# Kernel optimization log

Hardware: AMD Instinct MI355X
Metric: run time of the kernel (lower is better)

Reference implementation:

```python
import jax, jax.numpy as jnp
import numpy as np

DIM = 512
DIM_HEAD = 64
HEADS = 8
INNER = DIM_HEAD * HEADS  # 512
OUT_DIM = DIM
PB_ALPHA = 128.0
EPS = 1e-5
SCALE = DIM_HEAD ** (-0.5) / PB_ALPHA


def layer_norm(x, g):
    mean = jnp.mean(x, axis=-1, keepdims=True)
    var = jnp.mean(jnp.square(x - mean), axis=-1, keepdims=True)  # unbiased=False
    return (x - mean) * jax.lax.rsqrt(var + EPS) * g


def setup_inputs() -> dict:
    key = jax.random.key(0)
    ks = jax.random.split(key, 6)
    b, n, r = 4, 64, 256
    x = jax.random.normal(ks[0], (b, n, r, DIM), dtype=jnp.float32)
    g_norm = jnp.ones((DIM,), dtype=jnp.float32)
    W_q = jax.random.normal(ks[1], (DIM, INNER), dtype=jnp.float32) * (DIM ** -0.5)
    W_kv = jax.random.normal(ks[2], (DIM, 2 * DIM_HEAD), dtype=jnp.float32) * (DIM ** -0.5)
    W_out = jax.random.normal(ks[3], (INNER, OUT_DIM), dtype=jnp.float32) * (INNER ** -0.5)
    g_out = jnp.ones((OUT_DIM,), dtype=jnp.float32)
    return {"x": x, "g_norm": g_norm, "W_q": W_q, "W_kv": W_kv, "W_out": W_out, "g_out": g_out}


def reference(x, g_norm, W_q, W_kv, W_out, g_out):
    b, n, r, _ = x.shape
    xn = layer_norm(x, g_norm)                      # [b,n,r,dim]
    q = xn @ W_q                                    # [b,n,r,h*d]
    kv = xn @ W_kv                                  # context defaults to x
    k, v = jnp.split(kv, 2, axis=-1)                # [b,n,r,d] each, shared over heads
    q = q.reshape(b, n, r, HEADS, DIM_HEAD).transpose(0, 1, 3, 2, 4)  # b n h i d
    q = q * SCALE
    sim = jnp.einsum('bnhid,bnjd->bnhij', q, k)
    sim = (sim - jax.lax.stop_gradient(jnp.max(sim, axis=-1, keepdims=True))) * PB_ALPHA
    attn = jax.nn.softmax(sim, axis=-1)
    out = jnp.einsum('bnhij,bnjd->bnhid', attn, v)  # b n h i d
    out = out.transpose(0, 1, 3, 2, 4).reshape(b, n, r, INNER)  # b n i (h d)
    out = out @ W_out
    return layer_norm(out, g_out)
```

## Files before the change

kernel.cpp:

```cpp
#include <hip/hip_runtime.h>
#include <stdint.h>


#define DIM   512
#define DHEAD 64
#define RLEN  256
#define TOK   65536

typedef __bf16 bf16;
typedef __bf16 bf16x4 __attribute__((ext_vector_type(4)));
typedef __bf16 bf16x8 __attribute__((ext_vector_type(8)));
typedef float  f32x4  __attribute__((ext_vector_type(4)));
typedef short  s16x4  __attribute__((ext_vector_type(4)));

__device__ __forceinline__ f32x4 mfma16(bf16x8 a, bf16x8 b, f32x4 c) {
  return __builtin_amdgcn_mfma_f32_16x16x32_bf16(a, b, c, 0, 0, 0);
}
__device__ __forceinline__ f32x4 mfma_k16(bf16x4 a, bf16x4 b, f32x4 c) {
#if __has_builtin(__builtin_amdgcn_mfma_f32_16x16x16bf16_1k)
  return __builtin_amdgcn_mfma_f32_16x16x16bf16_1k(
      __builtin_bit_cast(s16x4, a), __builtin_bit_cast(s16x4, b), c, 0, 0, 0);
#else
  f32x4 d = c;
  asm volatile("v_mfma_f32_16x16x16_bf16 %0, %1, %2, %0"
               : "+v"(d) : "v"(a), "v"(b));
  return d;
#endif
}
__device__ __forceinline__ f32x4 fzero4() {
  f32x4 z; z[0] = z[1] = z[2] = z[3] = 0.f; return z;
}
__device__ __forceinline__ void gload_lds16(const void* g, void* l) {
  __builtin_amdgcn_global_load_lds(
      (const __attribute__((address_space(1))) void*)g,
      (__attribute__((address_space(3))) void*)l, 16, 0, 0);
}

__global__ __launch_bounds__(256) void k_prep_ln(
    const float* __restrict__ Wq, const float* __restrict__ Wkv,
    const float* __restrict__ Wout,
    const float* __restrict__ x, const float* __restrict__ gnorm,
    bf16* __restrict__ wall, bf16* __restrict__ woutt, bf16* __restrict__ xn) {
  if (blockIdx.x < 144) {
    __shared__ bf16 tile[64][72];
    const int b = blockIdx.x, tid = threadIdx.x;
    const float* src; bf16* dst; int srcN, kt, nt;
    if (b < 64)       { src = Wq;   dst = wall;  srcN = 512; kt = b >> 3;        nt = b & 7; }
    else if (b < 128) { src = Wout; dst = woutt; srcN = 512; kt = (b - 64) >> 3; nt = (b - 64) & 7; }
    else              { src = Wkv;  dst = wall + (size_t)512 * DIM; srcN = 128;
                        kt = (b - 128) >> 1; nt = (b - 128) & 1; }
    const int k0 = kt * 64, n0 = nt * 64;
    #pragma unroll
    for (int i = 0; i < 4; ++i) {
      int idx = i * 256 + tid;
      int r = idx >> 4, c4 = (idx & 15) * 4;
      float4 v = *(const float4*)(src + (size_t)(k0 + r) * srcN + n0 + c4);
      tile[r][c4 + 0] = (bf16)v.x;
      tile[r][c4 + 1] = (bf16)v.y;
      tile[r][c4 + 2] = (bf16)v.z;
      tile[r][c4 + 3] = (bf16)v.w;
    }
    __syncthreads();
    #pragma unroll
    for (int i = 0; i < 2; ++i) {
      int idx = i * 256 + tid;
      int n = idx >> 3, c = (idx & 7) * 8;
      bf16x8 o;
      #pragma unroll
      for (int j = 0; j < 8; ++j) o[j] = tile[c + j][n];
      *(bf16x8*)(dst + (size_t)(n0 + n) * DIM + k0 + c) = o;
    }
    return;
  }
  const int lane = threadIdx.x & 63;
  const int gw = (blockIdx.x - 144) * 4 + (threadIdx.x >> 6);
  float gv[8];
  #pragma unroll
  for (int j = 0; j < 8; ++j) gv[j] = gnorm[lane * 8 + j];
  #pragma unroll
  for (int i = 0; i < 8; ++i) {
    size_t row = (size_t)gw * 8 + i;
    const float4* xp = (const float4*)(x + row * DIM + lane * 8);
    float4 v0 = xp[0], v1 = xp[1];
    float s  = v0.x + v0.y + v0.z + v0.w + v1.x + v1.y + v1.z + v1.w;
    float sq = v0.x*v0.x + v0.y*v0.y + v0.z*v0.z + v0.w*v0.w
             + v1.x*v1.x + v1.y*v1.y + v1.z*v1.z + v1.w*v1.w;
    #pragma unroll
    for (int d = 1; d < 64; d <<= 1) { s += __shfl_xor(s, d); sq += __shfl_xor(sq, d); }
    float mean = s * (1.f / 512.f);
    float var  = sq * (1.f / 512.f) - mean * mean;
    float rs   = rsqrtf(var + 1e-5f);
    bf16x8 o;
    o[0] = (bf16)((v0.x - mean) * rs * gv[0]);
    o[1] = (bf16)((v0.y - mean) * rs * gv[1]);
    o[2] = (bf16)((v0.z - mean) * rs * gv[2]);
    o[3] = (bf16)((v0.w - mean) * rs * gv[3]);
    o[4] = (bf16)((v1.x - mean) * rs * gv[4]);
    o[5] = (bf16)((v1.y - mean) * rs * gv[5]);
    o[6] = (bf16)((v1.z - mean) * rs * gv[6]);
    o[7] = (bf16)((v1.w - mean) * rs * gv[7]);
    *(bf16x8*)(xn + row * DIM + lane * 8) = o;
  }
}

__global__ __launch_bounds__(256) void k_gemm_qkv(
    const bf16* __restrict__ xn, const bf16* __restrict__ wall,
    bf16* __restrict__ qbuf, bf16* __restrict__ kbuf, bf16* __restrict__ vtbuf) {
  __shared__ bf16 sa[2][128 * 32];
  __shared__ bf16 sb[2][128 * 32];
  const int t = threadIdx.x, wave = t >> 6, lane = t & 63;
  const int l15 = lane & 15, g = lane >> 4;
  const int wm = wave >> 1, wn = wave & 1;
  int wg = (blockIdx.x & 7) * 320 + (blockIdx.x >> 3);
  const int bm = wg / 5, bn = wg % 5;
  const char* Abase = (const char*)(xn   + (size_t)bm * 128 * DIM);
  const char* Bbase = (const char*)(wall + (size_t)bn * 128 * DIM);
  const int srow0 = wave * 16 + (lane >> 2);
  const int skb   = (lane & 3) * 16;

  #pragma unroll
  for (int c = 0; c < 2; ++c) {
    int row = c * 64 + srow0;
    int kb = skb ^ ((row & 3) << 4);
    gload_lds16(Abase + (size_t)row * 1024 + kb, (char*)&sa[0][0] + c * 4096 + wave * 1024);
    gload_lds16(Bbase + (size_t)row * 1024 + kb, (char*)&sb[0][0] + c * 4096 + wave * 1024);
  }
  __syncthreads();

  f32x4 acc[4][4];
  #pragma unroll
  for (int mi = 0; mi < 4; ++mi)
    #pragma unroll
    for (int ni = 0; ni < 4; ++ni) acc[mi][ni] = fzero4();

  #pragma unroll 2
  for (int step = 0; step < 16; ++step) {
    const int cur = step & 1;
    if (step < 15) {
      int kk2 = (step + 1) * 64;
      #pragma unroll
      for (int c = 0; c < 2; ++c) {
        int row = c * 64 + srow0;
        int kb = skb ^ ((row & 3) << 4);
        gload_lds16(Abase + (size_t)row * 1024 + kk2 + kb,
                    (char*)&sa[cur ^ 1][0] + c * 4096 + wave * 1024);
        gload_lds16(Bbase + (size_t)row * 1024 + kk2 + kb,
                    (char*)&sb[cur ^ 1][0] + c * 4096 + wave * 1024);
      }
    }
    bf16x8 a[4], b[4];
    #pragma unroll
    for (int mi = 0; mi < 4; ++mi) {
      int row = wm * 64 + mi * 16 + l15;
      a[mi] = *(const bf16x8*)((const char*)&sa[cur][0] + row * 64 + ((g * 16) ^ ((row & 3) << 4)));
    }
    #pragma unroll
    for (int ni = 0; ni < 4; ++ni) {
      int row = wn * 64 + ni * 16 + l15;
      b[ni] = *(const bf16x8*)((const char*)&sb[cur][0] + row * 64 + ((g * 16) ^ ((row & 3) << 4)));
    }
    #pragma unroll
    for (int mi = 0; mi < 4; ++mi)
      #pragma unroll
      for (int ni = 0; ni < 4; ++ni)
        acc[mi][ni] = mfma16(a[mi], b[ni], acc[mi][ni]);
    __syncthreads();
  }

  const float QSC = 0.1803368801f;
  #pragma unroll
  for (int ni = 0; ni < 4; ++ni) {
    int col0 = bn * 128 + wn * 64 + ni * 16;
    if (col0 < 512) {
      bf16* dst = qbuf + col0 + l15;
      #pragma unroll
      for (int mi = 0; mi < 4; ++mi)
        #pragma unroll
        for (int jj = 0; jj < 4; ++jj) {
          size_t row = (size_t)bm * 128 + wm * 64 + mi * 16 + g * 4 + jj;
          dst[row * DIM] = (bf16)(acc[mi][ni][jj] * QSC);
        }
    } else if (col0 < 576) {
      bf16* dst = kbuf + (col0 - 512) + l15;
      #pragma unroll
      for (int mi = 0; mi < 4; ++mi)
        #pragma unroll
        for (int jj = 0; jj < 4; ++jj) {
          size_t row = (size_t)bm * 128 + wm * 64 + mi * 16 + g * 4 + jj;
          dst[row * DHEAD] = (bf16)acc[mi][ni][jj];
        }
    } else {
      int d = col0 - 576 + l15;
      #pragma unroll
      for (int mi = 0; mi < 4; ++mi) {
        size_t row = (size_t)bm * 128 + wm * 64 + mi * 16 + g * 4;
        int bnr = (int)(row >> 8), kv = (int)(row & 255);
        bf16x4 v4;
        v4[0] = (bf16)acc[mi][ni][0]; v4[1] = (bf16)acc[mi][ni][1];
        v4[2] = (bf16)acc[mi][ni][2]; v4[3] = (bf16)acc[mi][ni][3];
        *(bf16x4*)(vtbuf + (size_t)bnr * 16384 + (size_t)d * 256 + kv) = v4;
      }
    }
  }
}

__global__ __launch_bounds__(512) void k_out_fused(
    const bf16* __restrict__ abuf, const bf16* __restrict__ woutt,
    const float* __restrict__ gout, float* __restrict__ out) {
  __shared__ bf16 sa[2][64 * 32];
  __shared__ bf16 sb[2][512 * 32];
  __shared__ float2 part[64][4];
  __shared__ float2 stats[64];
  const int t = threadIdx.x, wave = t >> 6, lane = t & 63;
  const int l15 = lane & 15, g = lane >> 4;
  const int wm = wave >> 2, wn = wave & 3;
  int wg = (blockIdx.x & 7) * 128 + (blockIdx.x >> 3);
  const size_t row0 = (size_t)wg * 64;
  const char* Abase = (const char*)(abuf + row0 * DIM);
  const int nsub = wave * 16 + (lane >> 2);
  const int skb  = (lane & 3) * 16;

  #pragma unroll
  for (int c = 0; c < 4; ++c) {
    int row = c * 128 + nsub;
    int kb = skb ^ ((row & 3) << 4);
    gload_lds16((const char*)(woutt + (size_t)row * DIM) + kb,
                (char*)&sb[0][0] + c * 8192 + wave * 1024);
  }
  if (t < 256) {
    int kb = skb ^ ((nsub & 3) << 4);
    gload_lds16(Abase + (size_t)nsub * 1024 + kb,
                (char*)&sa[0][0] + wave * 1024 + (lane & 63) * 16);
  }
  __syncthreads();

  f32x4 acc[2][8];
  #pragma unroll
  for (int mi = 0; mi < 2; ++mi)
    #pragma unroll
    for (int ni = 0; ni < 8; ++ni) acc[mi][ni] = fzero4();

  #pragma unroll 2
  for (int step = 0; step < 16; ++step) {
    const int cur = step & 1;
    if (step < 15) {
      int kk2 = (step + 1) * 64;
      #pragma unroll
      for (int c = 0; c < 4; ++c) {
        int row = c * 128 + nsub;
        int kb = skb ^ ((row & 3) << 4);
        gload_lds16((const char*)(woutt + (size_t)row * DIM) + kk2 + kb,
                    (char*)&sb[cur ^ 1][0] + c * 8192 + wave * 1024);
      }
      if (t < 256) {
        int kb = skb ^ ((nsub & 3) << 4);
        gload_lds16(Abase + (size_t)nsub * 1024 + kk2 + kb,
                    (char*)&sa[cur ^ 1][0] + wave * 1024 + lane * 16);
      }
    }
    bf16x8 a[2];
    #pragma unroll
    for (int mi = 0; mi < 2; ++mi) {
      int row = wm * 32 + mi * 16 + l15;
      a[mi] = *(const bf16x8*)((const char*)&sa[cur][0] + row * 64 + ((g * 16) ^ ((row & 3) << 4)));
    }
    #pragma unroll
    for (int ni = 0; ni < 8; ++ni) {
      int row = wn * 128 + ni * 16 + l15;
      bf16x8 b = *(const bf16x8*)((const char*)&sb[cur][0] + row * 64 + ((g * 16) ^ ((row & 3) << 4)));
      acc[0][ni] = mfma16(a[0], b, acc[0][ni]);
      acc[1][ni] = mfma16(a[1], b, acc[1][ni]);
    }
    __syncthreads();
  }

  #pragma unroll
  for (int mi = 0; mi < 2; ++mi)
    #pragma unroll
    for (int jj = 0; jj < 4; ++jj) {
      float s = 0.f, q = 0.f;
      #pragma unroll
      for (int ni = 0; ni < 8; ++ni) {
        float v = acc[mi][ni][jj];
        s += v; q += v * v;
      }
      s += __shfl_xor(s, 1); q += __shfl_xor(q, 1);
      s += __shfl_xor(s, 2); q += __shfl_xor(q, 2);
      s += __shfl_xor(s, 4); q += __shfl_xor(q, 4);
      s += __shfl_xor(s, 8); q += __shfl_xor(q, 8);
      if (l15 == 0) part[wm * 32 + mi * 16 + g * 4 + jj][wn] = make_float2(s, q);
    }
  __syncthreads();
  if (t < 64) {
    float S = 0.f, Q = 0.f;
    #pragma unroll
    for (int w = 0; w < 4; ++w) { S += part[t][w].x; Q += part[t][w].y; }
    float mean = S * (1.f / 512.f);
    float var  = Q * (1.f / 512.f) - mean * mean;
    stats[t] = make_float2(mean, rsqrtf(var + 1e-5f));
  }
  __syncthreads();

  #pragma unroll
  for (int mi = 0; mi < 2; ++mi)
    #pragma unroll
    for (int ni = 0; ni < 8; ++ni) {
      int col = wn * 128 + ni * 16 + l15;
      float gg = gout[col];
      #pragma unroll
      for (int jj = 0; jj < 4; ++jj) {
        int row = wm * 32 + mi * 16 + g * 4 + jj;
        float2 st = stats[row];
        out[(row0 + row) * DIM + col] = (acc[mi][ni][jj] - st.x) * st.y * gg;
      }
    }
}

__global__ __launch_bounds__(512, 2) void k_attn(
    bf16* __restrict__ qbuf, const bf16* __restrict__ kbuf,
    const bf16* __restrict__ vtbuf) {
  __shared__ char lds[256 * 144 + 64 * 528];
  char* lk  = lds;
  char* lvt = lds + 256 * 144;
  const int t = threadIdx.x, lane = t & 63;
  const int l15 = lane & 15, g = lane >> 4;
  int wg = (blockIdx.x & 7) * 256 + (blockIdx.x >> 3);
  const int bn = wg >> 3, h = wg & 7;
  const size_t tok0 = (size_t)bn * RLEN;
  const int m0 = (t >> 6) * 32;

  bf16x8 aq[2][2];
  {
    const bf16* qb = qbuf + (tok0 + m0 + l15) * DIM + h * DHEAD + g * 8;
    #pragma unroll
    for (int qh = 0; qh < 2; ++qh)
      #pragma unroll
      for (int ks = 0; ks < 2; ++ks)
        aq[qh][ks] = *(const bf16x8*)(qb + (size_t)qh * 16 * DIM + ks * 32);
  }
  {
    const bf16* ksrc = kbuf + tok0 * DHEAD;
    const bf16* vsrc = vtbuf + (size_t)bn * (64 * 256);
    bf16x8 kr[4], vr[4];
    #pragma unroll
    for (int i = 0; i < 4; ++i) kr[i] = *(const bf16x8*)(ksrc + (i * 512 + t) * 8);
    #pragma unroll
    for (int i = 0; i < 4; ++i) vr[i] = *(const bf16x8*)(vsrc + (i * 512 + t) * 8);
    #pragma unroll
    for (int i = 0; i < 4; ++i) {
      int off = i * 512 + t;
      *(bf16x8*)(lk + (off >> 3) * 144 + (off & 7) * 16) = kr[i];
    }
    #pragma unroll
    for (int i = 0; i < 4; ++i) {
      int off = i * 512 + t;
      *(bf16x8*)(lvt + (off >> 5) * 528 + (off & 31) * 16) = vr[i];
    }
  }
  __syncthreads();

  const char* bk_base = lk  + l15 * 144 + g * 16;
  const char* bv_base = lvt + l15 * 528 + g * 8;

  f32x4 o2[2][4];
  #pragma unroll
  for (int qh = 0; qh < 2; ++qh)
    #pragma unroll
    for (int di = 0; di < 4; ++di) o2[qh][di] = fzero4();
  float lsum0 = 0.f, lsum1 = 0.f;

  __builtin_amdgcn_s_setprio(1);
  #pragma unroll
  for (int f = 0; f < 16; ++f) {
    bf16x8 bk0 = *(const bf16x8*)(bk_base + f * 2304);
    bf16x8 bk1 = *(const bf16x8*)(bk_base + f * 2304 + 64);
    f32x4 s0 = mfma16(bk0, aq[0][0], fzero4());
    s0 = mfma16(bk1, aq[0][1], s0);
    f32x4 s1 = mfma16(bk0, aq[1][0], fzero4());
    s1 = mfma16(bk1, aq[1][1], s1);
    float p00 = exp2f(s0[0]), p01 = exp2f(s0[1]);
    float p02 = exp2f(s0[2]), p03 = exp2f(s0[3]);
    float p10 = exp2f(s1[0]), p11 = exp2f(s1[1]);
    float p12 = exp2f(s1[2]), p13 = exp2f(s1[3]);
    lsum0 += (p00 + p01) + (p02 + p03);
    lsum1 += (p10 + p11) + (p12 + p13);
    bf16x4 pk0, pk1;
    pk0[0] = (bf16)p00; pk0[1] = (bf16)p01; pk0[2] = (bf16)p02; pk0[3] = (bf16)p03;
    pk1[0] = (bf16)p10; pk1[1] = (bf16)p11; pk1[2] = (bf16)p12; pk1[3] = (bf16)p13;
    #pragma unroll
    for (int di = 0; di < 4; ++di) {
      bf16x4 bv = *(const bf16x4*)(bv_base + di * 8448 + f * 32);
      o2[0][di] = mfma_k16(pk0, bv, o2[0][di]);
      o2[1][di] = mfma_k16(pk1, bv, o2[1][di]);
    }
  }
  __builtin_amdgcn_s_setprio(0);

  float linv[2];
  lsum0 += __shfl_xor(lsum0, 16); lsum0 += __shfl_xor(lsum0, 32);
  lsum1 += __shfl_xor(lsum1, 16); lsum1 += __shfl_xor(lsum1, 32);
  linv[0] = 1.0f / lsum0;
  linv[1] = 1.0f / lsum1;

  #pragma unroll
  for (int qh = 0; qh < 2; ++qh)
    #pragma unroll
    for (int jj = 0; jj < 4; ++jj) {
      float inv = __shfl(linv[qh], 4 * g + jj);
      size_t row = tok0 + m0 + qh * 16 + 4 * g + jj;
      #pragma unroll
      for (int di = 0; di < 4; ++di)
        qbuf[row * DIM + h * DHEAD + di * 16 + l15] = (bf16)(o2[qh][di][jj] * inv);
    }
}

extern "C" void kernel_launch(void* const* d_in, const int* in_sizes, int n_in,
                              void* d_out, int out_size, void* d_ws, size_t ws_size,
                              hipStream_t stream) {
  const float* x     = (const float*)d_in[0];
  const float* gnorm = (const float*)d_in[1];
  const float* Wq    = (const float*)d_in[2];
  const float* Wkv   = (const float*)d_in[3];
  const float* Wout  = (const float*)d_in[4];
  const float* gout  = (const float*)d_in[5];
  float* out = (float*)d_out;
  char* ws = (char*)d_ws;
  bf16* wall  = (bf16*)(ws);
  bf16* woutt = (bf16*)(ws + 655360);
  bf16* xnbuf = (bf16*)(ws + 1179648);
  bf16* qbuf  = (bf16*)(ws + 1179648 + (size_t)TOK * DIM * 2);
  bf16* kbuf  = (bf16*)((char*)qbuf + (size_t)TOK * DIM * 2);
  bf16* vtbuf = (bf16*)((char*)kbuf + (size_t)TOK * DHEAD * 2);

  k_prep_ln  <<<dim3(2192), dim3(256), 0, stream>>>(Wq, Wkv, Wout, x, gnorm,
                                                    wall, woutt, xnbuf);
  k_gemm_qkv <<<dim3(2560), dim3(256), 0, stream>>>(xnbuf, wall, qbuf, kbuf, vtbuf);
  k_attn     <<<dim3(2048), dim3(512), 0, stream>>>(qbuf, kbuf, vtbuf);
  k_out_fused<<<dim3(1024), dim3(512), 0, stream>>>(qbuf, woutt, gout, out);
}
```

Baseline: 236.6 us.

## Process four heads per attention block and change LDS swizzle pattern

```diff
diff --git a/kernel.cpp b/kernel.cpp
--- a/kernel.cpp
+++ b/kernel.cpp
@@ -6,6 +6,7 @@
 #define DHEAD 64
 #define RLEN  256
 #define TOK   65536
+#define SWZ(row) ((((row) >> 1) & 3) << 4)
 
 typedef __bf16 bf16;
 typedef __bf16 bf16x4 __attribute__((ext_vector_type(4)));
@@ -121,7 +122,7 @@
   #pragma unroll
   for (int c = 0; c < 2; ++c) {
     int row = c * 64 + srow0;
-    int kb = skb ^ ((row & 3) << 4);
+    int kb = skb ^ SWZ(row);
     gload_lds16(Abase + (size_t)row * 1024 + kb, (char*)&sa[0][0] + c * 4096 + wave * 1024);
     gload_lds16(Bbase + (size_t)row * 1024 + kb, (char*)&sb[0][0] + c * 4096 + wave * 1024);
   }
@@ -141,7 +142,7 @@
       #pragma unroll
       for (int c = 0; c < 2; ++c) {
         int row = c * 64 + srow0;
-        int kb = skb ^ ((row & 3) << 4);
+        int kb = skb ^ SWZ(row);
         gload_lds16(Abase + (size_t)row * 1024 + kk2 + kb,
                     (char*)&sa[cur ^ 1][0] + c * 4096 + wave * 1024);
         gload_lds16(Bbase + (size_t)row * 1024 + kk2 + kb,
@@ -152,12 +153,12 @@
     #pragma unroll
     for (int mi = 0; mi < 4; ++mi) {
       int row = wm * 64 + mi * 16 + l15;
-      a[mi] = *(const bf16x8*)((const char*)&sa[cur][0] + row * 64 + ((g * 16) ^ ((row & 3) << 4)));
+      a[mi] = *(const bf16x8*)((const char*)&sa[cur][0] + row * 64 + ((g * 16) ^ SWZ(row)));
     }
     #pragma unroll
     for (int ni = 0; ni < 4; ++ni) {
       int row = wn * 64 + ni * 16 + l15;
-      b[ni] = *(const bf16x8*)((const char*)&sb[cur][0] + row * 64 + ((g * 16) ^ ((row & 3) << 4)));
+      b[ni] = *(const bf16x8*)((const char*)&sb[cur][0] + row * 64 + ((g * 16) ^ SWZ(row)));
     }
     #pragma unroll
     for (int mi = 0; mi < 4; ++mi)
@@ -223,12 +224,12 @@
   #pragma unroll
   for (int c = 0; c < 4; ++c) {
     int row = c * 128 + nsub;
-    int kb = skb ^ ((row & 3) << 4);
+    int kb = skb ^ SWZ(row);
     gload_lds16((const char*)(woutt + (size_t)row * DIM) + kb,
                 (char*)&sb[0][0] + c * 8192 + wave * 1024);
   }
   if (t < 256) {
-    int kb = skb ^ ((nsub & 3) << 4);
+    int kb = skb ^ SWZ(nsub);
     gload_lds16(Abase + (size_t)nsub * 1024 + kb,
                 (char*)&sa[0][0] + wave * 1024 + (lane & 63) * 16);
   }
@@ -248,12 +249,12 @@
       #pragma unroll
       for (int c = 0; c < 4; ++c) {
         int row = c * 128 + nsub;
-        int kb = skb ^ ((row & 3) << 4);
+        int kb = skb ^ SWZ(row);
         gload_lds16((const char*)(woutt + (size_t)row * DIM) + kk2 + kb,
                     (char*)&sb[cur ^ 1][0] + c * 8192 + wave * 1024);
       }
       if (t < 256) {
-        int kb = skb ^ ((nsub & 3) << 4);
+        int kb = skb ^ SWZ(nsub);
         gload_lds16(Abase + (size_t)nsub * 1024 + kk2 + kb,
                     (char*)&sa[cur ^ 1][0] + wave * 1024 + lane * 16);
       }
@@ -262,12 +263,12 @@
     #pragma unroll
     for (int mi = 0; mi < 2; ++mi) {
       int row = wm * 32 + mi * 16 + l15;
-      a[mi] = *(const bf16x8*)((const char*)&sa[cur][0] + row * 64 + ((g * 16) ^ ((row & 3) << 4)));
+      a[mi] = *(const bf16x8*)((const char*)&sa[cur][0] + row * 64 + ((g * 16) ^ SWZ(row)));
     }
     #pragma unroll
     for (int ni = 0; ni < 8; ++ni) {
       int row = wn * 128 + ni * 16 + l15;
-      bf16x8 b = *(const bf16x8*)((const char*)&sb[cur][0] + row * 64 + ((g * 16) ^ ((row & 3) << 4)));
+      bf16x8 b = *(const bf16x8*)((const char*)&sb[cur][0] + row * 64 + ((g * 16) ^ SWZ(row)));
       acc[0][ni] = mfma16(a[0], b, acc[0][ni]);
       acc[1][ni] = mfma16(a[1], b, acc[1][ni]);
     }
@@ -324,20 +325,11 @@
   char* lvt = lds + 256 * 144;
   const int t = threadIdx.x, lane = t & 63;
   const int l15 = lane & 15, g = lane >> 4;
-  int wg = (blockIdx.x & 7) * 256 + (blockIdx.x >> 3);
-  const int bn = wg >> 3, h = wg & 7;
+  int wg = (blockIdx.x & 7) * 64 + (blockIdx.x >> 3);
+  const int bn = wg >> 1, h0 = (wg & 1) * 4;
   const size_t tok0 = (size_t)bn * RLEN;
   const int m0 = (t >> 6) * 32;
 
-  bf16x8 aq[2][2];
-  {
-    const bf16* qb = qbuf + (tok0 + m0 + l15) * DIM + h * DHEAD + g * 8;
-    #pragma unroll
-    for (int qh = 0; qh < 2; ++qh)
-      #pragma unroll
-      for (int ks = 0; ks < 2; ++ks)
-        aq[qh][ks] = *(const bf16x8*)(qb + (size_t)qh * 16 * DIM + ks * 32);
-  }
   {
     const bf16* ksrc = kbuf + tok0 * DHEAD;
     const bf16* vsrc = vtbuf + (size_t)bn * (64 * 256);
@@ -361,57 +353,72 @@
 
   const char* bk_base = lk  + l15 * 144 + g * 16;
   const char* bv_base = lvt + l15 * 528 + g * 8;
-
-  f32x4 o2[2][4];
-  #pragma unroll
-  for (int qh = 0; qh < 2; ++qh)
-    #pragma unroll
-    for (int di = 0; di < 4; ++di) o2[qh][di] = fzero4();
-  float lsum0 = 0.f, lsum1 = 0.f;
-
-  __builtin_amdgcn_s_setprio(1);
-  #pragma unroll
-  for (int f = 0; f < 16; ++f) {
-    bf16x8 bk0 = *(const bf16x8*)(bk_base + f * 2304);
-    bf16x8 bk1 = *(const bf16x8*)(bk_base + f * 2304 + 64);
-    f32x4 s0 = mfma16(bk0, aq[0][0], fzero4());
-    s0 = mfma16(bk1, aq[0][1], s0);
-    f32x4 s1 = mfma16(bk0, aq[1][0], fzero4());
-    s1 = mfma16(bk1, aq[1][1], s1);
-    float p00 = exp2f(s0[0]), p01 = exp2f(s0[1]);
-    float p02 = exp2f(s0[2]), p03 = exp2f(s0[3]);
-    float p10 = exp2f(s1[0]), p11 = exp2f(s1[1]);
-    float p12 = exp2f(s1[2]), p13 = exp2f(s1[3]);
-    lsum0 += (p00 + p01) + (p02 + p03);
-    lsum1 += (p10 + p11) + (p12 + p13);
-    bf16x4 pk0, pk1;
-    pk0[0] = (bf16)p00; pk0[1] = (bf16)p01; pk0[2] = (bf16)p02; pk0[3] = (bf16)p03;
-    pk1[0] = (bf16)p10; pk1[1] = (bf16)p11; pk1[2] = (bf16)p12; pk1[3] = (bf16)p13;
-    #pragma unroll
-    for (int di = 0; di < 4; ++di) {
-      bf16x4 bv = *(const bf16x4*)(bv_base + di * 8448 + f * 32);
-      o2[0][di] = mfma_k16(pk0, bv, o2[0][di]);
-      o2[1][di] = mfma_k16(pk1, bv, o2[1][di]);
-    }
-  }
-  __builtin_amdgcn_s_setprio(0);
-
-  float linv[2];
-  lsum0 += __shfl_xor(lsum0, 16); lsum0 += __shfl_xor(lsum0, 32);
-  lsum1 += __shfl_xor(lsum1, 16); lsum1 += __shfl_xor(lsum1, 32);
-  linv[0] = 1.0f / lsum0;
-  linv[1] = 1.0f / lsum1;
-
-  #pragma unroll
-  for (int qh = 0; qh < 2; ++qh)
-    #pragma unroll
-    for (int jj = 0; jj < 4; ++jj) {
-      float inv = __shfl(linv[qh], 4 * g + jj);
-      size_t row = tok0 + m0 + qh * 16 + 4 * g + jj;
-      #pragma unroll
-      for (int di = 0; di < 4; ++di)
-        qbuf[row * DIM + h * DHEAD + di * 16 + l15] = (bf16)(o2[qh][di][jj] * inv);
-    }
+  const bf16* qrow = qbuf + (tok0 + m0 + l15) * DIM + g * 8;
+
+  #pragma unroll
+  for (int hi = 0; hi < 4; ++hi) {
+    const int h = h0 + hi;
+    bf16x8 aq[2][2];
+    {
+      const bf16* qb = qrow + h * DHEAD;
+      #pragma unroll
+      for (int qh = 0; qh < 2; ++qh)
+        #pragma unroll
+        for (int ks = 0; ks < 2; ++ks)
+          aq[qh][ks] = *(const bf16x8*)(qb + (size_t)qh * 16 * DIM + ks * 32);
+    }
+
+    f32x4 o2[2][4];
+    #pragma unroll
+    for (int qh = 0; qh < 2; ++qh)
+      #pragma unroll
+      for (int di = 0; di < 4; ++di) o2[qh][di] = fzero4();
+    float lsum0 = 0.f, lsum1 = 0.f;
+
+    __builtin_amdgcn_s_setprio(1);
+    #pragma unroll
+    for (int f = 0; f < 16; ++f) {
+      bf16x8 bk0 = *(const bf16x8*)(bk_base + f * 2304);
+      bf16x8 bk1 = *(const bf16x8*)(bk_base + f * 2304 + 64);
+      f32x4 s0 = mfma16(bk0, aq[0][0], fzero4());
+      s0 = mfma16(bk1, aq[0][1], s0);
+      f32x4 s1 = mfma16(bk0, aq[1][0], fzero4());
+      s1 = mfma16(bk1, aq[1][1], s1);
+      float p00 = exp2f(s0[0]), p01 = exp2f(s0[1]);
+      float p02 = exp2f(s0[2]), p03 = exp2f(s0[3]);
+      float p10 = exp2f(s1[0]), p11 = exp2f(s1[1]);
+      float p12 = exp2f(s1[2]), p13 = exp2f(s1[3]);
+      lsum0 += (p00 + p01) + (p02 + p03);
+      lsum1 += (p10 + p11) + (p12 + p13);
+      bf16x4 pk0, pk1;
+      pk0[0] = (bf16)p00; pk0[1] = (bf16)p01; pk0[2] = (bf16)p02; pk0[3] = (bf16)p03;
+      pk1[0] = (bf16)p10; pk1[1] = (bf16)p11; pk1[2] = (bf16)p12; pk1[3] = (bf16)p13;
+      #pragma unroll
+      for (int di = 0; di < 4; ++di) {
+        bf16x4 bv = *(const bf16x4*)(bv_base + di * 8448 + f * 32);
+        o2[0][di] = mfma_k16(pk0, bv, o2[0][di]);
+        o2[1][di] = mfma_k16(pk1, bv, o2[1][di]);
+      }
+    }
+    __builtin_amdgcn_s_setprio(0);
+
+    float linv[2];
+    lsum0 += __shfl_xor(lsum0, 16); lsum0 += __shfl_xor(lsum0, 32);
+    lsum1 += __shfl_xor(lsum1, 16); lsum1 += __shfl_xor(lsum1, 32);
+    linv[0] = 1.0f / lsum0;
+    linv[1] = 1.0f / lsum1;
+
+    #pragma unroll
+    for (int qh = 0; qh < 2; ++qh)
+      #pragma unroll
+      for (int jj = 0; jj < 4; ++jj) {
+        float inv = __shfl(linv[qh], 4 * g + jj);
+        size_t row = tok0 + m0 + qh * 16 + 4 * g + jj;
+        #pragma unroll
+        for (int di = 0; di < 4; ++di)
+          qbuf[row * DIM + h * DHEAD + di * 16 + l15] = (bf16)(o2[qh][di][jj] * inv);
+      }
+  }
 }
 
 extern "C" void kernel_launch(void* const* d_in, const int* in_sizes, int n_in,
@@ -435,6 +442,6 @@
   k_prep_ln  <<<dim3(2192), dim3(256), 0, stream>>>(Wq, Wkv, Wout, x, gnorm,
                                                     wall, woutt, xnbuf);
   k_gemm_qkv <<<dim3(2560), dim3(256), 0, stream>>>(xnbuf, wall, qbuf, kbuf, vtbuf);
-  k_attn     <<<dim3(2048), dim3(512), 0, stream>>>(qbuf, kbuf, vtbuf);
+  k_attn     <<<dim3(512),  dim3(512), 0, stream>>>(qbuf, kbuf, vtbuf);
   k_out_fused<<<dim3(1024), dim3(512), 0, stream>>>(qbuf, woutt, gout, out);
 }
```

Result: no change. 235.6 us (-0.4%).
